# Kernel optimization log

Measured on AMD Instinct MI355X. Metric: run time of the kernel, lower is better.

Reference implementation:

```python
import jax, jax.numpy as jnp
import numpy as np

B, T, C, D = 4, 2048, 1024, 64

def setup_inputs() -> dict:
    key = jax.random.key(0)
    ks = jax.random.split(key, 7)
    s = 1.0 / np.sqrt(C)
    return {
        "x":  jax.random.normal(ks[0], (B, T, C), dtype=jnp.float32),
        "Wq": jax.random.uniform(ks[1], (C, D), jnp.float32, -s, s),
        "bq": jax.random.uniform(ks[2], (D,),  jnp.float32, -s, s),
        "Wk": jax.random.uniform(ks[3], (C, D), jnp.float32, -s, s),
        "bk": jax.random.uniform(ks[4], (D,),  jnp.float32, -s, s),
        "Wv": jax.random.uniform(ks[5], (C, D), jnp.float32, -s, s),
        "bv": jax.random.uniform(ks[6], (D,),  jnp.float32, -s, s),
    }

def reference(x, Wq, bq, Wk, bk, Wv, bv):
    # QKV projections: [B,T,C] @ [C,D] -> [B,T,D]
    Q = jnp.einsum('btc,cd->btd', x, Wq) + bq
    K = jnp.einsum('btc,cd->btd', x, Wk) + bk
    V = jnp.einsum('btc,cd->btd', x, Wv) + bv
    scale = 1.0 / jnp.sqrt(jnp.float32(D))
    wei = jnp.einsum('bqd,bkd->bqk', Q, K) * scale  # [B,T,T]
    causal = jnp.tril(jnp.ones((T, T), dtype=bool))
    wei = jnp.where(causal, wei, jnp.float32(-1e9))  # masked_fill, not -inf
    wei = jax.nn.softmax(wei, axis=-1)
    return jnp.einsum('bqk,bkd->bqd', wei, V)  # [B,T,D]
```

## Files before the change

kernel.cpp:

```cpp
#include <hip/hip_runtime.h>
#include <stdint.h>

#define B_  4
#define T_  2048
#define C_  1024
#define D_  64

typedef float  f32x4  __attribute__((ext_vector_type(4)));
typedef float  f32x16 __attribute__((ext_vector_type(16)));
typedef short  s16x8  __attribute__((ext_vector_type(8)));

#define QSCALE 0.18033688011112042f

static __device__ __forceinline__ uint32_t f2bf(float f) {
  uint32_t u = __builtin_bit_cast(uint32_t, f);
  u += 0x7FFFu + ((u >> 16) & 1u);
  return u >> 16;
}
static __device__ __forceinline__ uint32_t pack2bf(float a, float b) {
  return f2bf(a) | (f2bf(b) << 16);
}

__global__ __launch_bounds__(256) void wconv_kernel(
    const float* __restrict__ Wq, const float* __restrict__ bq,
    const float* __restrict__ Wk, const float* __restrict__ bk,
    const float* __restrict__ Wv, const float* __restrict__ bv,
    uint16_t* __restrict__ Wp, float* __restrict__ biascat) {
  const int g = blockIdx.x * 256 + threadIdx.x;
  const int s32   = g / 768;
  const int rem   = g - s32 * 768;
  const int ntile = rem >> 6;
  const int l     = rem & 63;
  const int mrow  = l & 15, u = l >> 4;
  const int n     = ntile * 16 + mrow;
  const int mat   = n >> 6, col = n & 63;
  const float* W  = (mat == 0) ? Wq : ((mat == 1) ? Wk : Wv);
  const float  s  = (mat == 0) ? QSCALE : 1.0f;
  const int c0    = s32 * 32 + u * 8;
  float v[8];
#pragma unroll
  for (int j = 0; j < 8; ++j) v[j] = W[(size_t)(c0 + j) * D_ + col] * s;
  uint4 st;
  st.x = pack2bf(v[0], v[1]);
  st.y = pack2bf(v[2], v[3]);
  st.z = pack2bf(v[4], v[5]);
  st.w = pack2bf(v[6], v[7]);
  *reinterpret_cast<uint4*>(Wp + (size_t)g * 8) = st;
  if (g < 192) {
    float bb;
    if (g < 64)       bb = bq[g] * QSCALE;
    else if (g < 128) bb = bk[g - 64];
    else              bb = bv[g - 128];
    biascat[g] = bb;
  }
}

__global__ __launch_bounds__(256) void proj_kernel(
    const float* __restrict__ x, const uint16_t* __restrict__ Wp,
    const float* __restrict__ biascat,
    uint16_t* __restrict__ Qbf, uint16_t* __restrict__ Kbf,
    uint16_t* __restrict__ Vtile) {
  __shared__ __align__(16) uint16_t xt[2][16 * 132];
  __shared__ __align__(16) uint16_t tbuf[4][16 * 28];
  const int tid  = threadIdx.x;
  const int wave = tid >> 6;
  const int lane = tid & 63;
  const int mrow = lane & 15;
  const int u    = lane >> 4;
  const int m0   = blockIdx.x * 16;
  const int srow = tid >> 4, scol = tid & 15;

  const float* xg = x + (size_t)(m0 + srow) * C_ + scol * 4;

  f32x4 acc[3];
#pragma unroll
  for (int i = 0; i < 3; ++i)
#pragma unroll
    for (int r = 0; r < 4; ++r) acc[i][r] = 0.f;

  float4 xv0 = *reinterpret_cast<const float4*>(xg);
  float4 xv1 = *reinterpret_cast<const float4*>(xg + 64);
  {
    uint2 w0, w1;
    w0.x = pack2bf(xv0.x, xv0.y);  w0.y = pack2bf(xv0.z, xv0.w);
    w1.x = pack2bf(xv1.x, xv1.y);  w1.y = pack2bf(xv1.z, xv1.w);
    *reinterpret_cast<uint2*>(&xt[0][srow * 132 + scol * 4])      = w0;
    *reinterpret_cast<uint2*>(&xt[0][srow * 132 + scol * 4 + 64]) = w1;
  }
  __syncthreads();

  for (int s = 0; s < 8; ++s) {
    const int cur = s & 1;
    if (s < 7) {
      xv0 = *reinterpret_cast<const float4*>(xg + (s + 1) * 128);
      xv1 = *reinterpret_cast<const float4*>(xg + (s + 1) * 128 + 64);
    }
#pragma unroll
    for (int step = 0; step < 4; ++step) {
      const int s32 = s * 4 + step;
      s16x8 bf = *reinterpret_cast<const s16x8*>(
          &xt[cur][mrow * 132 + step * 32 + u * 8]);
      const uint16_t* wb = Wp + ((size_t)(s32 * 12 + wave * 3) * 64 + lane) * 8;
      s16x8 a0 = *reinterpret_cast<const s16x8*>(wb);
      s16x8 a1 = *reinterpret_cast<const s16x8*>(wb + 64 * 8);
      s16x8 a2 = *reinterpret_cast<const s16x8*>(wb + 128 * 8);
      acc[0] = __builtin_amdgcn_mfma_f32_16x16x32_bf16(a0, bf, acc[0], 0, 0, 0);
      acc[1] = __builtin_amdgcn_mfma_f32_16x16x32_bf16(a1, bf, acc[1], 0, 0, 0);
      acc[2] = __builtin_amdgcn_mfma_f32_16x16x32_bf16(a2, bf, acc[2], 0, 0, 0);
    }
    if (s < 7) {
      uint2 w0, w1;
      w0.x = pack2bf(xv0.x, xv0.y);  w0.y = pack2bf(xv0.z, xv0.w);
      w1.x = pack2bf(xv1.x, xv1.y);  w1.y = pack2bf(xv1.z, xv1.w);
      *reinterpret_cast<uint2*>(&xt[cur ^ 1][srow * 132 + scol * 4])      = w0;
      *reinterpret_cast<uint2*>(&xt[cur ^ 1][srow * 132 + scol * 4 + 64]) = w1;
      __syncthreads();
    }
  }

  const int bb  = m0 >> 11;
  const int mm  = m0 & (T_ - 1);
#pragma unroll
  for (int nt = 0; nt < 3; ++nt) {
    const int nb = wave * 48 + nt * 16;
    uint16_t vals[4];
#pragma unroll
    for (int r = 0; r < 4; ++r)
      vals[r] = (uint16_t)f2bf(acc[nt][r] + biascat[nb + u * 4 + r]);
    if (nb >= 128) {
      const int tl   = mm >> 5;
      const int toff = (mm & 31) + mrow;
#pragma unroll
      for (int r = 0; r < 4; ++r) {
        int vrow = nb - 128 + u * 4 + r;
        Vtile[(((size_t)bb * 64 + tl) * 64 + vrow) * 32 + toff] = vals[r];
      }
    } else {
#pragma unroll
      for (int r = 0; r < 4; ++r)
        tbuf[wave][mrow * 28 + u * 4 + r] = vals[r];
      const int row = lane >> 2, qtr = lane & 3;
      uint2 v = *reinterpret_cast<const uint2*>(&tbuf[wave][row * 28 + qtr * 4]);
      uint16_t* dst = (nb < 64) ? (Qbf + nb) : (Kbf + (nb - 64));
      *reinterpret_cast<uint2*>(dst + (size_t)(m0 + row) * D_ + qtr * 4) = v;
    }
  }
}

__global__ __launch_bounds__(256) void attn_kernel(
    const uint16_t* __restrict__ Qbf, const uint16_t* __restrict__ Kbf,
    const uint16_t* __restrict__ Vtile, float* __restrict__ partial,
    float* __restrict__ lpart) {
  __shared__ float wpart[4 * 2048];
  __shared__ float lw[128];

  const int tid  = threadIdx.x;
  const int wave = tid >> 6;
  const int lane = tid & 63;
  const int ql   = lane & 31;
  const int hi   = lane >> 5;

  const int blk = blockIdx.x;
  const int b   = (blk & 7) >> 1;
  const int j   = 2 * (blk >> 3) + (blk & 1);

  int a_ = 0;
  while (8 * (a_ + 1) * (a_ + 2) <= j) ++a_;
  const int off = j - 8 * a_ * (a_ + 1);
  const int r_  = off / (a_ + 1);
  const int ch  = off - r_ * (a_ + 1);
  const int qt  = 16 * a_ + r_;
  const int c16 = ch * 16;
  const int qb  = qt * 32;
  const int tmax = min(c16 + 15, qt);
  const int pj  = b * 160 + j;

  const uint16_t* Qb = Qbf + (size_t)b * T_ * D_;
  const uint16_t* Kb = Kbf + (size_t)b * T_ * D_;

  const uint16_t* qg = Qb + (size_t)(qb + ql) * D_ + hi * 8;
  s16x8 qf[4];
#pragma unroll
  for (int c = 0; c < 4; ++c)
    qf[c] = *reinterpret_cast<const s16x8*>(qg + c * 16);

  f32x16 aco[2];
#pragma unroll
  for (int i = 0; i < 2; ++i)
#pragma unroll
    for (int r = 0; r < 16; ++r) aco[i][r] = 0.f;
  float lacc = 0.f;

  auto load_tile = [&](int t, s16x8* kf, s16x8* vf) {
    const uint16_t* kg = Kb + (size_t)(t * 32 + ql) * D_ + hi * 8;
#pragma unroll
    for (int c = 0; c < 4; ++c)
      kf[c] = *reinterpret_cast<const s16x8*>(kg + c * 16);
    const uint16_t* vg = Vtile + ((size_t)(b * 64 + t) * 64 + ql) * 32 + hi * 8;
    vf[0] = *reinterpret_cast<const s16x8*>(vg);
    vf[1] = *reinterpret_cast<const s16x8*>(vg + 16);
    vf[2] = *reinterpret_cast<const s16x8*>(vg + 1024);
    vf[3] = *reinterpret_cast<const s16x8*>(vg + 1024 + 16);
  };

  auto compute = [&](int t, const s16x8* kf, const s16x8* vf) {
    f32x16 sacc;
#pragma unroll
    for (int r = 0; r < 16; ++r) sacc[r] = 0.f;
#pragma unroll
    for (int c = 0; c < 4; ++c)
      sacc = __builtin_amdgcn_mfma_f32_32x32x16_bf16(kf[c], qf[c], sacc, 0, 0, 0);
    if (t == qt) {
#pragma unroll
      for (int r = 0; r < 16; ++r) {
        const int koff = (r & 3) + 8 * (r >> 2) + 4 * hi;
        sacc[r] = (koff > ql) ? -1e30f : sacc[r];
      }
    }
    float p[16];
#pragma unroll
    for (int r = 0; r < 16; ++r) p[r] = __builtin_amdgcn_exp2f(sacc[r]);
    float s01 = (p[0] + p[1]) + (p[2] + p[3]);
    float s23 = (p[4] + p[5]) + (p[6] + p[7]);
    float s45 = (p[8] + p[9]) + (p[10] + p[11]);
    float s67 = (p[12] + p[13]) + (p[14] + p[15]);
    lacc += (s01 + s23) + (s45 + s67);

    uint32_t A0 = pack2bf(p[0], p[1]),  A1 = pack2bf(p[2], p[3]);
    uint32_t B0 = pack2bf(p[4], p[5]),  B1 = pack2bf(p[6], p[7]);
    uint32_t C0 = pack2bf(p[8], p[9]),  C1 = pack2bf(p[10], p[11]);
    uint32_t D0 = pack2bf(p[12], p[13]), D1 = pack2bf(p[14], p[15]);
    uint32_t r0 = (uint32_t)__shfl_xor((int)(hi ? A0 : B0), 32, 64);
    uint32_t r1 = (uint32_t)__shfl_xor((int)(hi ? A1 : B1), 32, 64);
    uint32_t r2 = (uint32_t)__shfl_xor((int)(hi ? C0 : D0), 32, 64);
    uint32_t r3 = (uint32_t)__shfl_xor((int)(hi ? C1 : D1), 32, 64);
    union { uint32_t u[4]; s16x8 v; } pf0, pf1;
    pf0.u[0] = hi ? r0 : A0;  pf0.u[1] = hi ? r1 : A1;
    pf0.u[2] = hi ? B0 : r0;  pf0.u[3] = hi ? B1 : r1;
    pf1.u[0] = hi ? r2 : C0;  pf1.u[1] = hi ? r3 : C1;
    pf1.u[2] = hi ? D0 : r2;  pf1.u[3] = hi ? D1 : r3;
    aco[0] = __builtin_amdgcn_mfma_f32_32x32x16_bf16(vf[0], pf0.v, aco[0], 0, 0, 0);
    aco[1] = __builtin_amdgcn_mfma_f32_32x32x16_bf16(vf[2], pf0.v, aco[1], 0, 0, 0);
    aco[0] = __builtin_amdgcn_mfma_f32_32x32x16_bf16(vf[1], pf1.v, aco[0], 0, 0, 0);
    aco[1] = __builtin_amdgcn_mfma_f32_32x32x16_bf16(vf[3], pf1.v, aco[1], 0, 0, 0);
  };

  {
    int t = c16 + wave;
    if (t <= tmax) {
      s16x8 kfA[4], vfA[4], kfB[4], vfB[4];
      load_tile(t, kfA, vfA);
      while (true) {
        int tn = t + 4;
        if (tn <= tmax) load_tile(tn, kfB, vfB);
        compute(t, kfA, vfA);
        if (tn > tmax) break;
        t = tn; tn = t + 4;
        if (tn <= tmax) load_tile(tn, kfA, vfA);
        compute(t, kfB, vfB);
        if (tn > tmax) break;
        t = tn;
      }
    }
  }

  lacc += __shfl_xor(lacc, 32, 64);

#pragma unroll
  for (int dm = 0; dm < 2; ++dm)
#pragma unroll
    for (int r = 0; r < 16; ++r)
      wpart[wave * 2048 + dm * 1024 + r * 64 + hi * 32 + ql] = aco[dm][r];
  if (hi == 0) lw[wave * 32 + ql] = lacc;
  __syncthreads();

  {
    const int base = tid * 8;
    float4 s0 = {0.f, 0.f, 0.f, 0.f}, s1 = {0.f, 0.f, 0.f, 0.f};
#pragma unroll
    for (int w = 0; w < 4; ++w) {
      const float* p = wpart + w * 2048 + base;
      float4 a = *reinterpret_cast<const float4*>(p);
      float4 c = *reinterpret_cast<const float4*>(p + 4);
      s0.x += a.x; s0.y += a.y; s0.z += a.z; s0.w += a.w;
      s1.x += c.x; s1.y += c.y; s1.z += c.z; s1.w += c.w;
    }
    float* pp = partial + (size_t)pj * 2048 + base;
    *reinterpret_cast<float4*>(pp)     = s0;
    *reinterpret_cast<float4*>(pp + 4) = s1;
    if (tid < 32) {
      float ls = (lw[tid] + lw[32 + tid]) + (lw[64 + tid] + lw[96 + tid]);
      lpart[(size_t)pj * 32 + tid] = ls;
    }
  }
}

__global__ __launch_bounds__(256) void reduce_kernel(
    const float* __restrict__ partial, const float* __restrict__ lpart,
    float* __restrict__ out) {
  __shared__ float trans[64 * 33];
  __shared__ float lbuf[32];
  const int blk = blockIdx.x;
  const int b   = blk >> 6;
  const int qt  = blk & 63;
  const int a_  = qt >> 4;
  const int nch = a_ + 1;
  const int pjb = b * 160 + 8 * a_ * (a_ + 1) + (qt & 15) * (a_ + 1);
  const int t   = threadIdx.x;

  if (t < 32) {
    float s = 0.f;
    for (int c = 0; c < nch; ++c) s += lpart[(size_t)(pjb + c) * 32 + t];
    lbuf[t] = 1.0f / s;
  }

  const int base = t * 8;
  float4 s0 = {0.f, 0.f, 0.f, 0.f}, s1 = {0.f, 0.f, 0.f, 0.f};
  for (int c = 0; c < nch; ++c) {
    const float* p = partial + (size_t)(pjb + c) * 2048 + base;
    float4 a = *reinterpret_cast<const float4*>(p);
    float4 d = *reinterpret_cast<const float4*>(p + 4);
    s0.x += a.x; s0.y += a.y; s0.z += a.z; s0.w += a.w;
    s1.x += d.x; s1.y += d.y; s1.z += d.z; s1.w += d.w;
  }
  const int dm = base >> 10, r = (base >> 6) & 15, hi = (base >> 5) & 1;
  const int ql0 = base & 31;
  const int d = dm * 32 + (r & 3) + 8 * (r >> 2) + 4 * hi;
  float* tr = &trans[d * 33 + ql0];
  tr[0] = s0.x; tr[1] = s0.y; tr[2] = s0.z; tr[3] = s0.w;
  tr[4] = s1.x; tr[5] = s1.y; tr[6] = s1.z; tr[7] = s1.w;
  __syncthreads();

  const int q  = t >> 3;
  const int dg = (t & 7) * 8;
  const float rinv = lbuf[q];
  float4 o0, o1;
  o0.x = trans[(dg + 0) * 33 + q] * rinv;
  o0.y = trans[(dg + 1) * 33 + q] * rinv;
  o0.z = trans[(dg + 2) * 33 + q] * rinv;
  o0.w = trans[(dg + 3) * 33 + q] * rinv;
  o1.x = trans[(dg + 4) * 33 + q] * rinv;
  o1.y = trans[(dg + 5) * 33 + q] * rinv;
  o1.z = trans[(dg + 6) * 33 + q] * rinv;
  o1.w = trans[(dg + 7) * 33 + q] * rinv;
  float* op = out + ((size_t)(b * T_ + qt * 32 + q)) * D_ + dg;
  *reinterpret_cast<float4*>(op)     = o0;
  *reinterpret_cast<float4*>(op + 4) = o1;
}

extern "C" void kernel_launch(void* const* d_in, const int* in_sizes, int n_in,
                              void* d_out, int out_size, void* d_ws, size_t ws_size,
                              hipStream_t stream) {
  (void)in_sizes; (void)n_in; (void)out_size; (void)ws_size;
  const float* x  = (const float*)d_in[0];
  const float* Wq = (const float*)d_in[1];
  const float* bq = (const float*)d_in[2];
  const float* Wk = (const float*)d_in[3];
  const float* bk = (const float*)d_in[4];
  const float* Wv = (const float*)d_in[5];
  const float* bv = (const float*)d_in[6];
  float* out = (float*)d_out;

  char* ws = (char*)d_ws;
  uint16_t* Wp      = (uint16_t*)(ws);
  float*    biascat = (float*)(ws + 393216);
  uint16_t* Qbf     = (uint16_t*)(ws + 394240);
  uint16_t* Kbf     = (uint16_t*)(ws + 1442816);
  uint16_t* Vtile   = (uint16_t*)(ws + 2491392);
  float*    partial = (float*)(ws + 3539968);
  float*    lpart   = (float*)(ws + 8782848);

  hipLaunchKernelGGL(wconv_kernel, dim3(96), dim3(256), 0, stream,
                     Wq, bq, Wk, bk, Wv, bv, Wp, biascat);
  hipLaunchKernelGGL(proj_kernel, dim3(512), dim3(256), 0, stream,
                     x, Wp, biascat, Qbf, Kbf, Vtile);
  hipLaunchKernelGGL(attn_kernel, dim3(640), dim3(256), 0, stream,
                     Qbf, Kbf, Vtile, partial, lpart);
  hipLaunchKernelGGL(reduce_kernel, dim3(256), dim3(256), 0, stream,
                     partial, lpart, out);
}
```

Before: 110.8 us.

## Split attention key chunks into 8-tile pieces and deepen x prefetch in projection

The attention work split changes from chunks of 16 key tiles to chunks of 8. This raises the block count from 640 to 1152 and shortens the longest per-block loop, for better load balance and occupancy on the causal triangle. The reduce kernel indexing and the partial-buffer layout are updated to match. Separately, the projection kernel now prefetches x two stages ahead using a double register buffer, to hide global-load latency. The costs are more partial-sum traffic and reduce work, plus extra registers in the projection kernel.

```diff
diff --git a/kernel.cpp b/kernel.cpp
--- a/kernel.cpp
+++ b/kernel.cpp
@@ -78,23 +78,24 @@
 #pragma unroll
     for (int r = 0; r < 4; ++r) acc[i][r] = 0.f;
 
-  float4 xv0 = *reinterpret_cast<const float4*>(xg);
-  float4 xv1 = *reinterpret_cast<const float4*>(xg + 64);
+  float4 rb[2][2];
   {
+    float4 a0 = *reinterpret_cast<const float4*>(xg);
+    float4 a1 = *reinterpret_cast<const float4*>(xg + 64);
     uint2 w0, w1;
-    w0.x = pack2bf(xv0.x, xv0.y);  w0.y = pack2bf(xv0.z, xv0.w);
-    w1.x = pack2bf(xv1.x, xv1.y);  w1.y = pack2bf(xv1.z, xv1.w);
+    w0.x = pack2bf(a0.x, a0.y);  w0.y = pack2bf(a0.z, a0.w);
+    w1.x = pack2bf(a1.x, a1.y);  w1.y = pack2bf(a1.z, a1.w);
     *reinterpret_cast<uint2*>(&xt[0][srow * 132 + scol * 4])      = w0;
     *reinterpret_cast<uint2*>(&xt[0][srow * 132 + scol * 4 + 64]) = w1;
   }
+  rb[0][0] = *reinterpret_cast<const float4*>(xg + 128);
+  rb[0][1] = *reinterpret_cast<const float4*>(xg + 192);
+  rb[1][0] = *reinterpret_cast<const float4*>(xg + 256);
+  rb[1][1] = *reinterpret_cast<const float4*>(xg + 320);
   __syncthreads();
 
   for (int s = 0; s < 8; ++s) {
     const int cur = s & 1;
-    if (s < 7) {
-      xv0 = *reinterpret_cast<const float4*>(xg + (s + 1) * 128);
-      xv1 = *reinterpret_cast<const float4*>(xg + (s + 1) * 128 + 64);
-    }
 #pragma unroll
     for (int step = 0; step < 4; ++step) {
       const int s32 = s * 4 + step;
@@ -110,10 +111,16 @@
     }
     if (s < 7) {
       uint2 w0, w1;
-      w0.x = pack2bf(xv0.x, xv0.y);  w0.y = pack2bf(xv0.z, xv0.w);
-      w1.x = pack2bf(xv1.x, xv1.y);  w1.y = pack2bf(xv1.z, xv1.w);
+      w0.x = pack2bf(rb[cur][0].x, rb[cur][0].y);
+      w0.y = pack2bf(rb[cur][0].z, rb[cur][0].w);
+      w1.x = pack2bf(rb[cur][1].x, rb[cur][1].y);
+      w1.y = pack2bf(rb[cur][1].z, rb[cur][1].w);
       *reinterpret_cast<uint2*>(&xt[cur ^ 1][srow * 132 + scol * 4])      = w0;
       *reinterpret_cast<uint2*>(&xt[cur ^ 1][srow * 132 + scol * 4 + 64]) = w1;
+      if (s + 3 < 8) {
+        rb[cur][0] = *reinterpret_cast<const float4*>(xg + (s + 3) * 128);
+        rb[cur][1] = *reinterpret_cast<const float4*>(xg + (s + 3) * 128 + 64);
+      }
       __syncthreads();
     }
   }
@@ -165,15 +172,15 @@
   const int j   = 2 * (blk >> 3) + (blk & 1);
 
   int a_ = 0;
-  while (8 * (a_ + 1) * (a_ + 2) <= j) ++a_;
-  const int off = j - 8 * a_ * (a_ + 1);
+  while (4 * (a_ + 1) * (a_ + 2) <= j) ++a_;
+  const int off = j - 4 * a_ * (a_ + 1);
   const int r_  = off / (a_ + 1);
   const int ch  = off - r_ * (a_ + 1);
-  const int qt  = 16 * a_ + r_;
-  const int c16 = ch * 16;
+  const int qt  = 8 * a_ + r_;
+  const int c8  = ch * 8;
   const int qb  = qt * 32;
-  const int tmax = min(c16 + 15, qt);
-  const int pj  = b * 160 + j;
+  const int tmax = min(c8 + 7, qt);
+  const int pj  = b * 288 + j;
 
   const uint16_t* Qb = Qbf + (size_t)b * T_ * D_;
   const uint16_t* Kb = Kbf + (size_t)b * T_ * D_;
@@ -246,7 +253,7 @@
   };
 
   {
-    int t = c16 + wave;
+    int t = c8 + wave;
     if (t <= tmax) {
       s16x8 kfA[4], vfA[4], kfB[4], vfB[4];
       load_tile(t, kfA, vfA);
@@ -303,9 +310,9 @@
   const int blk = blockIdx.x;
   const int b   = blk >> 6;
   const int qt  = blk & 63;
-  const int a_  = qt >> 4;
+  const int a_  = qt >> 3;
   const int nch = a_ + 1;
-  const int pjb = b * 160 + 8 * a_ * (a_ + 1) + (qt & 15) * (a_ + 1);
+  const int pjb = b * 288 + 4 * a_ * (a_ + 1) + (qt & 7) * (a_ + 1);
   const int t   = threadIdx.x;
 
   if (t < 32) {
@@ -368,13 +375,13 @@
   uint16_t* Kbf     = (uint16_t*)(ws + 1442816);
   uint16_t* Vtile   = (uint16_t*)(ws + 2491392);
   float*    partial = (float*)(ws + 3539968);
-  float*    lpart   = (float*)(ws + 8782848);
+  float*    lpart   = (float*)(ws + 12977152);
 
   hipLaunchKernelGGL(wconv_kernel, dim3(96), dim3(256), 0, stream,
                      Wq, bq, Wk, bk, Wv, bv, Wp, biascat);
   hipLaunchKernelGGL(proj_kernel, dim3(512), dim3(256), 0, stream,
                      x, Wp, biascat, Qbf, Kbf, Vtile);
-  hipLaunchKernelGGL(attn_kernel, dim3(640), dim3(256), 0, stream,
+  hipLaunchKernelGGL(attn_kernel, dim3(1152), dim3(256), 0, stream,
                      Qbf, Kbf, Vtile, partial, lpart);
   hipLaunchKernelGGL(reduce_kernel, dim3(256), dim3(256), 0, stream,
                      partial, lpart, out);
```

New measurement: 114.3 us. +3.2%, slower.

## Store Q/K/V in MFMA fragment-major layout for contiguous per-lane loads

Applied to the files above, without the earlier changes.

The projection kernel now writes Q, K and V into a fragment-ordered layout, where each 32-row tile holds 4 chunks of 64 lanes × 8 bf16. The attention kernel can then load each MFMA operand as one fully contiguous 1KB read per wave instead of strided row reads. This targets global-load coalescing in the attention inner loop. In exchange, the projection kernel's stores become more scattered, especially the 2-byte V stores.

```diff
diff --git a/kernel.cpp b/kernel.cpp
--- a/kernel.cpp
+++ b/kernel.cpp
@@ -58,8 +58,8 @@
 __global__ __launch_bounds__(256) void proj_kernel(
     const float* __restrict__ x, const uint16_t* __restrict__ Wp,
     const float* __restrict__ biascat,
-    uint16_t* __restrict__ Qbf, uint16_t* __restrict__ Kbf,
-    uint16_t* __restrict__ Vtile) {
+    uint16_t* __restrict__ Qfrag, uint16_t* __restrict__ Kfrag,
+    uint16_t* __restrict__ Vfrag) {
   __shared__ __align__(16) uint16_t xt[2][16 * 132];
   __shared__ __align__(16) uint16_t tbuf[4][16 * 28];
   const int tid  = threadIdx.x;
@@ -128,12 +128,16 @@
     for (int r = 0; r < 4; ++r)
       vals[r] = (uint16_t)f2bf(acc[nt][r] + biascat[nb + u * 4 + r]);
     if (nb >= 128) {
-      const int tl   = mm >> 5;
-      const int toff = (mm & 31) + mrow;
+      const int tg  = mm + mrow;
+      const int t   = tg >> 5, rem = tg & 31;
+      const int kc  = rem >> 4, hi2 = (rem >> 3) & 1, jj = rem & 7;
+      uint16_t* base = Vfrag + ((size_t)(bb * 64 + t)) * 2048;
 #pragma unroll
       for (int r = 0; r < 4; ++r) {
-        int vrow = nb - 128 + u * 4 + r;
-        Vtile[(((size_t)bb * 64 + tl) * 64 + vrow) * 32 + toff] = vals[r];
+        int d = nb - 128 + u * 4 + r;
+        int i = (d >> 5) * 2 + kc;
+        int l = hi2 * 32 + (d & 31);
+        base[i * 512 + l * 8 + jj] = vals[r];
       }
     } else {
 #pragma unroll
@@ -141,15 +145,21 @@
         tbuf[wave][mrow * 28 + u * 4 + r] = vals[r];
       const int row = lane >> 2, qtr = lane & 3;
       uint2 v = *reinterpret_cast<const uint2*>(&tbuf[wave][row * 28 + qtr * 4]);
-      uint16_t* dst = (nb < 64) ? (Qbf + nb) : (Kbf + (nb - 64));
-      *reinterpret_cast<uint2*>(dst + (size_t)(m0 + row) * D_ + qtr * 4) = v;
+      const int m  = m0 + row;
+      const int e0 = (nb & 63) + qtr * 4;
+      const int t  = (m & 2047) >> 5;
+      const int c  = e0 >> 4, hi2 = (e0 >> 3) & 1, j0 = e0 & 7;
+      uint16_t* dst = (nb < 64) ? Qfrag : Kfrag;
+      *reinterpret_cast<uint2*>(
+          dst + ((size_t)(bb * 64 + t)) * 2048 + c * 512 +
+          (hi2 * 32 + (m & 31)) * 8 + j0) = v;
     }
   }
 }
 
 __global__ __launch_bounds__(256) void attn_kernel(
-    const uint16_t* __restrict__ Qbf, const uint16_t* __restrict__ Kbf,
-    const uint16_t* __restrict__ Vtile, float* __restrict__ partial,
+    const uint16_t* __restrict__ Qfrag, const uint16_t* __restrict__ Kfrag,
+    const uint16_t* __restrict__ Vfrag, float* __restrict__ partial,
     float* __restrict__ lpart) {
   __shared__ float wpart[4 * 2048];
   __shared__ float lw[128];
@@ -171,18 +181,16 @@
   const int ch  = off - r_ * (a_ + 1);
   const int qt  = 16 * a_ + r_;
   const int c16 = ch * 16;
-  const int qb  = qt * 32;
   const int tmax = min(c16 + 15, qt);
   const int pj  = b * 160 + j;
 
-  const uint16_t* Qb = Qbf + (size_t)b * T_ * D_;
-  const uint16_t* Kb = Kbf + (size_t)b * T_ * D_;
-
-  const uint16_t* qg = Qb + (size_t)(qb + ql) * D_ + hi * 8;
   s16x8 qf[4];
-#pragma unroll
-  for (int c = 0; c < 4; ++c)
-    qf[c] = *reinterpret_cast<const s16x8*>(qg + c * 16);
+  {
+    const uint16_t* qg = Qfrag + ((size_t)(b * 64 + qt)) * 2048 + lane * 8;
+#pragma unroll
+    for (int c = 0; c < 4; ++c)
+      qf[c] = *reinterpret_cast<const s16x8*>(qg + c * 512);
+  }
 
   f32x16 aco[2];
 #pragma unroll
@@ -192,15 +200,14 @@
   float lacc = 0.f;
 
   auto load_tile = [&](int t, s16x8* kf, s16x8* vf) {
-    const uint16_t* kg = Kb + (size_t)(t * 32 + ql) * D_ + hi * 8;
+    const uint16_t* kg = Kfrag + ((size_t)(b * 64 + t)) * 2048 + lane * 8;
 #pragma unroll
     for (int c = 0; c < 4; ++c)
-      kf[c] = *reinterpret_cast<const s16x8*>(kg + c * 16);
-    const uint16_t* vg = Vtile + ((size_t)(b * 64 + t) * 64 + ql) * 32 + hi * 8;
-    vf[0] = *reinterpret_cast<const s16x8*>(vg);
-    vf[1] = *reinterpret_cast<const s16x8*>(vg + 16);
-    vf[2] = *reinterpret_cast<const s16x8*>(vg + 1024);
-    vf[3] = *reinterpret_cast<const s16x8*>(vg + 1024 + 16);
+      kf[c] = *reinterpret_cast<const s16x8*>(kg + c * 512);
+    const uint16_t* vg = Vfrag + ((size_t)(b * 64 + t)) * 2048 + lane * 8;
+#pragma unroll
+    for (int i = 0; i < 4; ++i)
+      vf[i] = *reinterpret_cast<const s16x8*>(vg + i * 512);
   };
 
   auto compute = [&](int t, const s16x8* kf, const s16x8* vf) {
@@ -364,18 +371,18 @@
   char* ws = (char*)d_ws;
   uint16_t* Wp      = (uint16_t*)(ws);
   float*    biascat = (float*)(ws + 393216);
-  uint16_t* Qbf     = (uint16_t*)(ws + 394240);
-  uint16_t* Kbf     = (uint16_t*)(ws + 1442816);
-  uint16_t* Vtile   = (uint16_t*)(ws + 2491392);
+  uint16_t* Qfrag   = (uint16_t*)(ws + 394240);
+  uint16_t* Kfrag   = (uint16_t*)(ws + 1442816);
+  uint16_t* Vfrag   = (uint16_t*)(ws + 2491392);
   float*    partial = (float*)(ws + 3539968);
   float*    lpart   = (float*)(ws + 8782848);
 
   hipLaunchKernelGGL(wconv_kernel, dim3(96), dim3(256), 0, stream,
                      Wq, bq, Wk, bk, Wv, bv, Wp, biascat);
   hipLaunchKernelGGL(proj_kernel, dim3(512), dim3(256), 0, stream,
-                     x, Wp, biascat, Qbf, Kbf, Vtile);
+                     x, Wp, biascat, Qfrag, Kfrag, Vfrag);
   hipLaunchKernelGGL(attn_kernel, dim3(640), dim3(256), 0, stream,
-                     Qbf, Kbf, Vtile, partial, lpart);
+                     Qfrag, Kfrag, Vfrag, partial, lpart);
   hipLaunchKernelGGL(reduce_kernel, dim3(256), dim3(256), 0, stream,
                      partial, lpart, out);
 }
```

Result: faster. 105.7 us (-4.6%).
